# Kernel tuning notes

Hardware: AMD Instinct MI355X
Metric: run time of the kernel (lower is better)

Reference implementation:

```python
import jax, jax.numpy as jnp
import numpy as np
from jax import lax

BATCH, SEQ, D_FSQ = 8, 4096, 4
D_MODEL, D_STATE, D_CONV, L, OUT = 256, 16, 4, 2, 2
D_INNER = 2 * D_MODEL  # expand=2
EPS = 1e-5


def setup_inputs() -> dict:
    key = jax.random.key(0)
    ks = jax.random.split(key, 10)
    s = 0.02
    return {
        "z_seq": jax.random.normal(ks[0], (BATCH, SEQ, D_FSQ), jnp.float32),
        "ip_w": jax.random.normal(ks[1], (D_MODEL, D_FSQ), jnp.float32) * s,
        "ip_b": jnp.zeros((D_MODEL,), jnp.float32),
        "norm_g": jnp.ones((L, D_MODEL), jnp.float32),
        "norm_b": jnp.zeros((L, D_MODEL), jnp.float32),
        "inproj_w": jax.random.normal(ks[2], (L, 2 * D_INNER, D_MODEL), jnp.float32) * s,
        "conv_w": jax.random.normal(ks[3], (L, D_INNER, D_CONV), jnp.float32) * s,
        "conv_b": jnp.zeros((L, D_INNER), jnp.float32),
        "xproj_w": jax.random.normal(ks[4], (L, 2 * D_STATE + 1, D_INNER), jnp.float32) * s,
        "dt_w": jax.random.normal(ks[5], (L, D_INNER), jnp.float32) * s,
        "dt_b": jnp.zeros((L, D_INNER), jnp.float32),
        "outproj_w": jax.random.normal(ks[6], (L, D_MODEL, D_INNER), jnp.float32) * s,
        "onorm_g": jnp.ones((D_MODEL,), jnp.float32),
        "onorm_b": jnp.zeros((D_MODEL,), jnp.float32),
        "op_w": jax.random.normal(ks[7], (OUT, D_MODEL), jnp.float32) * s,
        "op_b": jnp.zeros((OUT,), jnp.float32),
    }


def _layernorm(x, g, b):
    mu = jnp.mean(x, axis=-1, keepdims=True)
    var = jnp.mean(jnp.square(x - mu), axis=-1, keepdims=True)
    return (x - mu) * lax.rsqrt(var + EPS) * g + b


def _selective_scan(x, dt, Bm, Cm):
    # x, dt: [B,T,d_inner]; Bm, Cm: [B,T,d_state]
    A = -jnp.arange(1, D_STATE + 1, dtype=x.dtype)  # [d_state]

    def step(h, inp):
        x_t, dt_t, B_t, C_t = inp  # [B,di],[B,di],[B,ds],[B,ds]
        A_bar = jnp.exp(dt_t[:, :, None] * A)            # [B,di,ds]
        h = A_bar * h + (dt_t * x_t)[:, :, None] * B_t[:, None, :]
        y_t = jnp.einsum("bds,bs->bd", h, C_t)
        return h, y_t

    xs = (jnp.swapaxes(x, 0, 1), jnp.swapaxes(dt, 0, 1),
          jnp.swapaxes(Bm, 0, 1), jnp.swapaxes(Cm, 0, 1))
    h0 = jnp.zeros((x.shape[0], D_INNER, D_STATE), x.dtype)
    _, ys = lax.scan(step, h0, xs)
    return jnp.swapaxes(ys, 0, 1)  # [B,T,d_inner]


def _block(x, g, b, Wi, cw, cb, Wx, dw, db, Wo):
    res = x
    x = _layernorm(x, g, b)
    xz = x @ Wi.T                               # [B,T,2*d_inner]
    xp, z = xz[..., :D_INNER], xz[..., D_INNER:]
    # causal depthwise conv1d (padding=d_conv-1 then truncate == left pad)
    xc = lax.conv_general_dilated(
        jnp.swapaxes(xp, 1, 2), cw[:, None, :], window_strides=(1,),
        padding=[(D_CONV - 1, 0)], dimension_numbers=("NCH", "OIH", "NCH"),
        feature_group_count=D_INNER) + cb[None, :, None]
    xc = jax.nn.silu(jnp.swapaxes(xc, 1, 2))    # [B,T,d_inner]
    ssm = xc @ Wx.T                             # [B,T,2*ds+1]
    Bm = ssm[..., :D_STATE]
    Cm = ssm[..., D_STATE:2 * D_STATE]
    dt_raw = ssm[..., 2 * D_STATE:]             # [B,T,1]
    dt = jax.nn.softplus(dt_raw * dw + db)      # Linear(1, d_inner)
    y = _selective_scan(xc, dt, Bm, Cm)
    y = y * jax.nn.silu(z)
    y = y @ Wo.T
    return y + res


def reference(z_seq, ip_w, ip_b, norm_g, norm_b, inproj_w, conv_w, conv_b,
              xproj_w, dt_w, dt_b, outproj_w, onorm_g, onorm_b, op_w, op_b):
    x = z_seq @ ip_w.T + ip_b
    for l in range(L):
        x = _block(x, norm_g[l], norm_b[l], inproj_w[l], conv_w[l], conv_b[l],
                   xproj_w[l], dt_w[l], dt_b[l], outproj_w[l])
    x = _layernorm(x, onorm_g, onorm_b)
    return x @ op_w.T + op_b
```

## Files before the change

kernel.cpp:

```cpp
#include <hip/hip_runtime.h>
#include <cstddef>
#include <cstdint>

#define DEV __device__ __forceinline__

namespace {
constexpr int BATCH = 8;
constexpr int SEQL  = 4096;
constexpr int DM    = 256;
constexpr int DS    = 16;
constexpr int DI    = 512;
constexpr int NTOK  = BATCH * SEQL;
constexpr int TC    = 32;
constexpr int NCH   = SEQL / TC;
constexpr float EPSF = 1e-5f;

constexpr size_t OFF_X   = 0;
constexpr size_t OFF_XPB = OFF_X   + (size_t)NTOK * DM * 4;
constexpr size_t OFF_ZBB = OFF_XPB + (size_t)NTOK * DI * 2;
constexpr size_t OFF_XCB = OFF_ZBB + (size_t)NTOK * DI * 2;
constexpr size_t OFF_XLN = OFF_XCB + (size_t)NTOK * DI * 2;
constexpr size_t OFF_B   = OFF_XLN + (size_t)NTOK * DM * 2;
constexpr size_t OFF_C   = OFF_B   + (size_t)NTOK * DS * 4;
constexpr size_t OFF_DTR = OFF_C   + (size_t)NTOK * DS * 4;
constexpr size_t OFF_HE  = OFF_DTR + (size_t)NTOK * 4;
constexpr size_t OFF_DTC = OFF_HE  + (size_t)BATCH * DI * NCH * DS * 4;
constexpr size_t OFF_WBI = OFF_DTC + (size_t)BATCH * DI * NCH * 4;
constexpr size_t OFF_WBO = OFF_WBI + (size_t)2 * 2 * DI * DM * 2;
constexpr size_t OFF_WBX = OFF_WBO + (size_t)2 * DM * DI * 2;
constexpr size_t OFF_CWT = OFF_WBX + (size_t)2 * 48 * DI * 2;
constexpr size_t WBI_EL  = 2 * 2 * DI * DM;
constexpr size_t WBO_EL  = 2 * DM * DI;
}

typedef __attribute__((ext_vector_type(8))) short short8;
typedef __attribute__((ext_vector_type(4))) float f32x4;

DEV float sigmoidf_(float v) { return 1.0f / (1.0f + __expf(-v)); }
DEV float siluf_(float v)    { return v * sigmoidf_(v); }
DEV float b2f(unsigned short u) {
    union { unsigned int i; float f; } c; c.i = ((unsigned int)u) << 16; return c.f;
}
DEV float4 b4f(ushort4 u) {
    return make_float4(b2f(u.x), b2f(u.y), b2f(u.z), b2f(u.w));
}
DEV unsigned short f2b(float f) {
    union { float f; unsigned int i; } c; c.f = f;
    unsigned int lsb = (c.i >> 16) & 1u;
    c.i += 0x7fffu + lsb;
    return (unsigned short)(c.i >> 16);
}
DEV void dt_p_(float a, float& dt, float& p) {
    p = __builtin_amdgcn_rcpf(1.0f + __expf(a));
    dt = -__logf(p);
}
DEV void pows16(float p, float* pb) {
    float p2 = p * p, p4 = p2 * p2, p8 = p4 * p4;
    pb[0] = p;        pb[1] = p2;       pb[2] = p2 * p;      pb[3] = p4;
    pb[4] = p4 * p;   pb[5] = p4 * p2;  pb[6] = p4 * p2 * p; pb[7] = p8;
    pb[8] = p8 * p;   pb[9] = p8 * p2;  pb[10] = p8 * p2 * p; pb[11] = p8 * p4;
    pb[12] = p8 * p4 * p; pb[13] = p8 * p4 * p2; pb[14] = p8 * p4 * p2 * p; pb[15] = p8 * p8;
}
DEV void gload_lds16(const unsigned short* g, unsigned short* l) {
    __builtin_amdgcn_global_load_lds(
        (__attribute__((address_space(1))) void*)(g),
        (__attribute__((address_space(3))) void*)(l), 16, 0, 0);
}

__global__ void k_cvt(const float* __restrict__ src, unsigned short* __restrict__ dst, int n) {
    int g = (blockIdx.x * 256 + threadIdx.x) * 4;
    if (g >= n) return;
    float4 v = *(const float4*)(src + g);
    ushort4 o;
    o.x = f2b(v.x); o.y = f2b(v.y); o.z = f2b(v.z); o.w = f2b(v.w);
    *(ushort4*)(dst + g) = o;
}

__global__ void k_cvtx(const float* __restrict__ src, unsigned short* __restrict__ dst) {
    int idx = blockIdx.x * 256 + threadIdx.x;
    int l = idx / (48 * 512), r = (idx >> 9) % 48, cc = idx & 511;
    dst[idx] = (r < 33) ? f2b(src[(size_t)(l * 33 + r) * 512 + cc]) : (unsigned short)0;
}

__global__ void k_cvtc(const float* __restrict__ src, float* __restrict__ dst) {
    int idx = blockIdx.x * 256 + threadIdx.x;
    int l = idx >> 11, k = (idx >> 9) & 3, d = idx & 511;
    dst[idx] = src[(size_t)(l * DI + d) * 4 + k];
}

__global__ void k_inproj(const float* __restrict__ z, const float* __restrict__ w,
                         const float* __restrict__ bias, float* __restrict__ x) {
    int g = blockIdx.x * 256 + threadIdx.x;
    int i = g >> 8, m = g & 255;
    float4 zv = *(const float4*)(z + (size_t)i * 4);
    float4 wv = *(const float4*)(w + (size_t)m * 4);
    float r = bias[m];
    r = fmaf(zv.x, wv.x, r);
    r = fmaf(zv.y, wv.y, r);
    r = fmaf(zv.z, wv.z, r);
    r = fmaf(zv.w, wv.w, r);
    x[g] = r;
}

__global__ void k_lnrow(const float* __restrict__ x, const float* __restrict__ gam,
                        const float* __restrict__ bet, unsigned short* __restrict__ xln) {
    int lane = threadIdx.x & 63, wid = threadIdx.x >> 6;
    int i = blockIdx.x * 4 + wid;
    float4 v = *(const float4*)(x + (size_t)i * DM + lane * 4);
    float s = v.x + v.y + v.z + v.w;
    float q = v.x * v.x + v.y * v.y + v.z * v.z + v.w * v.w;
    #pragma unroll
    for (int m = 32; m; m >>= 1) { s += __shfl_xor(s, m, 64); q += __shfl_xor(q, m, 64); }
    float mu = s * (1.0f / DM);
    float rs = rsqrtf(q * (1.0f / DM) - mu * mu + EPSF);
    float4 g4 = *(const float4*)(gam + lane * 4);
    float4 b4 = *(const float4*)(bet + lane * 4);
    ushort4 o;
    o.x = f2b((v.x - mu) * rs * g4.x + b4.x);
    o.y = f2b((v.y - mu) * rs * g4.y + b4.y);
    o.z = f2b((v.z - mu) * rs * g4.z + b4.z);
    o.w = f2b((v.w - mu) * rs * g4.w + b4.w);
    *(ushort4*)(xln + (size_t)i * DM + lane * 4) = o;
}

__global__ __launch_bounds__(256) void k_gemm1(
    const unsigned short* __restrict__ A, const unsigned short* __restrict__ W,
    unsigned short* __restrict__ xpb, unsigned short* __restrict__ zbb) {
    __shared__ unsigned short As[128 * 32];
    __shared__ unsigned short Bs[128 * 32];
    int tid = threadIdx.x, lane = tid & 63, wid = tid >> 6;
    int tileN = blockIdx.x & 7, tileM = blockIdx.x >> 3;
    int i0 = tileM * 128, n0 = tileN * 128;
    f32x4 acc[4][4];
    #pragma unroll
    for (int mi = 0; mi < 4; mi++)
        #pragma unroll
        for (int ni = 0; ni < 4; ni++) acc[mi][ni] = (f32x4){0.f, 0.f, 0.f, 0.f};

    int srow = (wid << 5) + (lane >> 2);
    int sblk = lane & 3;
    const unsigned short* ga = A + (size_t)(i0 + srow) * 256 + sblk * 8;
    const unsigned short* gb = W + (size_t)(n0 + srow) * 256 + sblk * 8;
    unsigned short* la = As + (wid << 5) * 32;
    unsigned short* lb = Bs + (wid << 5) * 32;
    int ar = lane & 15, ab = lane >> 4;
    const short8* pa = (const short8*)(As + ((wid >> 1) * 64 + ar) * 32 + ab * 8);
    const short8* pb = (const short8*)(Bs + ((wid & 1) * 64 + ar) * 32 + ab * 8);

    for (int k0 = 0; k0 < 256; k0 += 32) {
        gload_lds16(ga + k0,            la);
        gload_lds16(ga + k0 + 16 * 256, la + 16 * 32);
        gload_lds16(gb + k0,            lb);
        gload_lds16(gb + k0 + 16 * 256, lb + 16 * 32);
        __syncthreads();
        short8 a[4], b[4];
        #pragma unroll
        for (int mi = 0; mi < 4; mi++) a[mi] = pa[mi * 64];
        #pragma unroll
        for (int ni = 0; ni < 4; ni++) b[ni] = pb[ni * 64];
        #pragma unroll
        for (int mi = 0; mi < 4; mi++)
            #pragma unroll
            for (int ni = 0; ni < 4; ni++)
                acc[mi][ni] = __builtin_amdgcn_mfma_f32_16x16x32_bf16(a[mi], b[ni], acc[mi][ni], 0, 0, 0);
        __syncthreads();
    }
    int wr = wid >> 1, wc = wid & 1;
    int rbase = i0 + wr * 64 + (lane >> 4) * 4;
    int cbase = n0 + wc * 64 + (lane & 15);
    unsigned short* dst = (n0 < 512) ? xpb : zbb;
    int coff = (n0 < 512) ? cbase : cbase - 512;
    #pragma unroll
    for (int mi = 0; mi < 4; mi++)
        #pragma unroll
        for (int ni = 0; ni < 4; ni++)
            #pragma unroll
            for (int j = 0; j < 4; j++)
                dst[(size_t)(rbase + mi * 16 + j) * 512 + coff + ni * 16] = f2b(acc[mi][ni][j]);
}

__global__ void k_conv(const unsigned short* __restrict__ xpb, const float* __restrict__ cwT,
                       const float* __restrict__ cb, unsigned short* __restrict__ xcb) {
    int g = blockIdx.x * 256 + threadIdx.x;
    int tg = g >> 7, dq = g & 127;
    int d = dq * 4;
    int i0 = tg * 8;
    float4 w0 = *(const float4*)(cwT + 0 * DI + d);
    float4 w1 = *(const float4*)(cwT + 1 * DI + d);
    float4 w2 = *(const float4*)(cwT + 2 * DI + d);
    float4 w3 = *(const float4*)(cwT + 3 * DI + d);
    float4 bi = *(const float4*)(cb + d);
    float4 x0, x1, x2;
    if ((i0 & (SEQL - 1)) != 0) {
        x0 = b4f(*(const ushort4*)(xpb + (size_t)(i0 - 3) * DI + d));
        x1 = b4f(*(const ushort4*)(xpb + (size_t)(i0 - 2) * DI + d));
        x2 = b4f(*(const ushort4*)(xpb + (size_t)(i0 - 1) * DI + d));
    } else {
        x0 = x1 = x2 = make_float4(0.f, 0.f, 0.f, 0.f);
    }
    #pragma unroll
    for (int tt = 0; tt < 8; tt++) {
        float4 xc = b4f(*(const ushort4*)(xpb + (size_t)(i0 + tt) * DI + d));
        float4 a = bi;
        a.x = fmaf(w0.x, x0.x, a.x); a.y = fmaf(w0.y, x0.y, a.y);
        a.z = fmaf(w0.z, x0.z, a.z); a.w = fmaf(w0.w, x0.w, a.w);
        a.x = fmaf(w1.x, x1.x, a.x); a.y = fmaf(w1.y, x1.y, a.y);
        a.z = fmaf(w1.z, x1.z, a.z); a.w = fmaf(w1.w, x1.w, a.w);
        a.x = fmaf(w2.x, x2.x, a.x); a.y = fmaf(w2.y, x2.y, a.y);
        a.z = fmaf(w2.z, x2.z, a.z); a.w = fmaf(w2.w, x2.w, a.w);
        a.x = fmaf(w3.x, xc.x, a.x); a.y = fmaf(w3.y, xc.y, a.y);
        a.z = fmaf(w3.z, xc.z, a.z); a.w = fmaf(w3.w, xc.w, a.w);
        ushort4 o;
        o.x = f2b(siluf_(a.x)); o.y = f2b(siluf_(a.y));
        o.z = f2b(siluf_(a.z)); o.w = f2b(siluf_(a.w));
        *(ushort4*)(xcb + (size_t)(i0 + tt) * DI + d) = o;
        x0 = x1; x1 = x2; x2 = xc;
    }
}

__global__ __launch_bounds__(256) void k_xprojm(
    const unsigned short* __restrict__ A, const unsigned short* __restrict__ W,
    float* __restrict__ Bm, float* __restrict__ Cm, float* __restrict__ dtr) {
    __shared__ unsigned short As[128 * 32];
    __shared__ unsigned short Bs[48 * 32];
    int tid = threadIdx.x, lane = tid & 63, wid = tid >> 6;
    int i0 = blockIdx.x * 128;
    f32x4 acc[2][3];
    #pragma unroll
    for (int mi = 0; mi < 2; mi++)
        #pragma unroll
        for (int ni = 0; ni < 3; ni++) acc[mi][ni] = (f32x4){0.f, 0.f, 0.f, 0.f};

    int srow = lane >> 2, sblk = lane & 3;
    const unsigned short* ga = A + (size_t)(i0 + (wid << 5) + srow) * 512 + sblk * 8;
    unsigned short* la = As + (wid << 5) * 32;
    const unsigned short* gb = W + (size_t)((wid << 4) + srow) * 512 + sblk * 8;
    unsigned short* lb = Bs + (wid << 4) * 32;
    int ar = lane & 15, ab = lane >> 4;

    for (int k0 = 0; k0 < 512; k0 += 32) {
        gload_lds16(ga + k0,            la);
        gload_lds16(ga + k0 + 16 * 512, la + 16 * 32);
        if (wid < 3) gload_lds16(gb + k0, lb);
        __syncthreads();
        short8 a[2], b[3];
        #pragma unroll
        for (int mi = 0; mi < 2; mi++)
            a[mi] = *(const short8*)(As + ((wid << 5) + mi * 16 + ar) * 32 + ab * 8);
        #pragma unroll
        for (int ni = 0; ni < 3; ni++)
            b[ni] = *(const short8*)(Bs + (ni * 16 + ar) * 32 + ab * 8);
        #pragma unroll
        for (int mi = 0; mi < 2; mi++)
            #pragma unroll
            for (int ni = 0; ni < 3; ni++)
                acc[mi][ni] = __builtin_amdgcn_mfma_f32_16x16x32_bf16(a[mi], b[ni], acc[mi][ni], 0, 0, 0);
        __syncthreads();
    }
    #pragma unroll
    for (int mi = 0; mi < 2; mi++)
        #pragma unroll
        for (int ni = 0; ni < 3; ni++)
            #pragma unroll
            for (int j = 0; j < 4; j++) {
                int row = i0 + (wid << 5) + mi * 16 + (lane >> 4) * 4 + j;
                int ng = ni * 16 + (lane & 15);
                float v = acc[mi][ni][j];
                if (ng < 16)       Bm[(size_t)row * DS + ng] = v;
                else if (ng < 32)  Cm[(size_t)row * DS + ng - 16] = v;
                else if (ng == 32) dtr[row] = v;
            }
}

__global__ __launch_bounds__(256, 4) void k_scan1(
    const unsigned short* __restrict__ xcb, const float* __restrict__ Bm,
    const float* __restrict__ dtr, const float* __restrict__ dw,
    const float* __restrict__ db, float* __restrict__ hend, float* __restrict__ dtc) {
    __shared__ float Bsh[TC][16];
    __shared__ float dtl[TC];
    int tid = threadIdx.x;
    int blk = blockIdx.x;
    int c = blk & (NCH - 1), b = blk >> 7;
    int d0 = tid * 2;
    int i0 = (b << 12) + c * TC;
    if (tid < TC) dtl[tid] = dtr[i0 + tid];
    if (tid < TC * 4) {
        int tt = tid >> 2, ss = (tid & 3) * 4;
        *(float4*)(&Bsh[tt][ss]) = *(const float4*)(Bm + (size_t)(i0 + tt) * DS + ss);
    }
    __syncthreads();
    float2 dwd = *(const float2*)(dw + d0);
    float2 dbd = *(const float2*)(db + d0);
    float h0[16], h1[16];
    #pragma unroll
    for (int s = 0; s < 16; s++) { h0[s] = 0.0f; h1[s] = 0.0f; }
    float dts0 = 0.0f, dts1 = 0.0f;
    for (int t = 0; t < TC; t++) {
        float dt0, p0, dt1, p1;
        dt_p_(fmaf(dtl[t], dwd.x, dbd.x), dt0, p0);
        dt_p_(fmaf(dtl[t], dwd.y, dbd.y), dt1, p1);
        dts0 += dt0; dts1 += dt1;
        ushort2 xv = *(const ushort2*)(xcb + (size_t)(i0 + t) * DI + d0);
        float dtx0 = dt0 * b2f(xv.x);
        float dtx1 = dt1 * b2f(xv.y);
        float Bv[16];
        *(float4*)(Bv + 0)  = *(const float4*)(&Bsh[t][0]);
        *(float4*)(Bv + 4)  = *(const float4*)(&Bsh[t][4]);
        *(float4*)(Bv + 8)  = *(const float4*)(&Bsh[t][8]);
        *(float4*)(Bv + 12) = *(const float4*)(&Bsh[t][12]);
        float pb[16];
        pows16(p0, pb);
        #pragma unroll
        for (int s = 0; s < 16; s++) h0[s] = fmaf(pb[s], h0[s], dtx0 * Bv[s]);
        pows16(p1, pb);
        #pragma unroll
        for (int s = 0; s < 16; s++) h1[s] = fmaf(pb[s], h1[s], dtx1 * Bv[s]);
    }
    size_t hb0 = ((size_t)(b * DI + d0) * NCH + c) * DS;
    #pragma unroll
    for (int s = 0; s < 16; s += 4) {
        *(float4*)(hend + hb0 + s)      = make_float4(h0[s], h0[s+1], h0[s+2], h0[s+3]);
        *(float4*)(hend + hb0 + DS * NCH + s) = make_float4(h1[s], h1[s+1], h1[s+2], h1[s+3]);
    }
    dtc[(size_t)(b * DI + d0) * NCH + c] = dts0;
    dtc[(size_t)(b * DI + d0 + 1) * NCH + c] = dts1;
}

__global__ void k_scan2(float* __restrict__ hend, const float* __restrict__ dtc) {
    int g = blockIdx.x * 256 + threadIdx.x;
    int s = g & 15, dd = (g >> 4) & 511, b = g >> 13;
    size_t base = (size_t)(b * DI + dd) * NCH;
    float hin = 0.0f;
    float kneg = -(float)(s + 1);
    #pragma unroll 4
    for (int c = 0; c < NCH; c++) {
        size_t a = (base + c) * DS + s;
        float tmp = hend[a];
        float pb = __expf(kneg * dtc[base + c]);
        hend[a] = hin;
        hin = fmaf(pb, hin, tmp);
    }
}

__global__ __launch_bounds__(256, 4) void k_scan3(
    const unsigned short* __restrict__ xcb, const float* __restrict__ Bm,
    const float* __restrict__ Cm, const float* __restrict__ dtr,
    const float* __restrict__ dw, const float* __restrict__ db,
    const float* __restrict__ hend, const unsigned short* __restrict__ zbb,
    unsigned short* __restrict__ ygb) {
    __shared__ float Bsh[TC][16];
    __shared__ float Csh[TC][16];
    __shared__ float dtl[TC];
    int tid = threadIdx.x;
    int blk = blockIdx.x;
    int c = blk & (NCH - 1), b = blk >> 7;
    int d0 = tid * 2;
    int i0 = (b << 12) + c * TC;
    if (tid < TC) dtl[tid] = dtr[i0 + tid];
    if (tid < TC * 4) {
        int tt = tid >> 2, ss = (tid & 3) * 4;
        *(float4*)(&Bsh[tt][ss]) = *(const float4*)(Bm + (size_t)(i0 + tt) * DS + ss);
    } else if (tid < TC * 8) {
        int q = tid - TC * 4;
        int tt = q >> 2, ss = (q & 3) * 4;
        *(float4*)(&Csh[tt][ss]) = *(const float4*)(Cm + (size_t)(i0 + tt) * DS + ss);
    }
    __syncthreads();
    float2 dwd = *(const float2*)(dw + d0);
    float2 dbd = *(const float2*)(db + d0);
    float h0[16], h1[16];
    size_t hb0 = ((size_t)(b * DI + d0) * NCH + c) * DS;
    #pragma unroll
    for (int s = 0; s < 16; s += 4) {
        *(float4*)(h0 + s) = *(const float4*)(hend + hb0 + s);
        *(float4*)(h1 + s) = *(const float4*)(hend + hb0 + DS * NCH + s);
    }
    for (int t = 0; t < TC; t++) {
        float dt0, p0, dt1, p1;
        dt_p_(fmaf(dtl[t], dwd.x, dbd.x), dt0, p0);
        dt_p_(fmaf(dtl[t], dwd.y, dbd.y), dt1, p1);
        size_t gi = (size_t)(i0 + t) * DI + d0;
        ushort2 xv = *(const ushort2*)(xcb + gi);
        float dtx0 = dt0 * b2f(xv.x);
        float dtx1 = dt1 * b2f(xv.y);
        float Bv[16], Cv[16];
        *(float4*)(Bv + 0)  = *(const float4*)(&Bsh[t][0]);
        *(float4*)(Bv + 4)  = *(const float4*)(&Bsh[t][4]);
        *(float4*)(Bv + 8)  = *(const float4*)(&Bsh[t][8]);
        *(float4*)(Bv + 12) = *(const float4*)(&Bsh[t][12]);
        *(float4*)(Cv + 0)  = *(const float4*)(&Csh[t][0]);
        *(float4*)(Cv + 4)  = *(const float4*)(&Csh[t][4]);
        *(float4*)(Cv + 8)  = *(const float4*)(&Csh[t][8]);
        *(float4*)(Cv + 12) = *(const float4*)(&Csh[t][12]);
        float pb[16];
        float y0 = 0.0f, y1 = 0.0f;
        pows16(p0, pb);
        #pragma unroll
        for (int s = 0; s < 16; s++) {
            h0[s] = fmaf(pb[s], h0[s], dtx0 * Bv[s]);
            y0 = fmaf(h0[s], Cv[s], y0);
        }
        pows16(p1, pb);
        #pragma unroll
        for (int s = 0; s < 16; s++) {
            h1[s] = fmaf(pb[s], h1[s], dtx1 * Bv[s]);
            y1 = fmaf(h1[s], Cv[s], y1);
        }
        ushort2 zv = *(const ushort2*)(zbb + gi);
        ushort2 o;
        o.x = f2b(y0 * siluf_(b2f(zv.x)));
        o.y = f2b(y1 * siluf_(b2f(zv.y)));
        *(ushort2*)(ygb + gi) = o;
    }
}

__global__ __launch_bounds__(256) void k_outproj(
    const unsigned short* __restrict__ A, const unsigned short* __restrict__ W,
    float* __restrict__ x) {
    __shared__ unsigned short As[128 * 32];
    __shared__ unsigned short Bs[128 * 32];
    int tid = threadIdx.x, lane = tid & 63, wid = tid >> 6;
    int tileN = blockIdx.x & 1, tileM = blockIdx.x >> 1;
    int i0 = tileM * 128, n0 = tileN * 128;
    f32x4 acc[4][4];
    #pragma unroll
    for (int mi = 0; mi < 4; mi++)
        #pragma unroll
        for (int ni = 0; ni < 4; ni++) acc[mi][ni] = (f32x4){0.f, 0.f, 0.f, 0.f};

    int srow = (wid << 5) + (lane >> 2);
    int sblk = lane & 3;
    const unsigned short* ga = A + (size_t)(i0 + srow) * 512 + sblk * 8;
    const unsigned short* gb = W + (size_t)(n0 + srow) * 512 + sblk * 8;
    unsigned short* la = As + (wid << 5) * 32;
    unsigned short* lb = Bs + (wid << 5) * 32;
    int ar = lane & 15, ab = lane >> 4;
    const short8* pa = (const short8*)(As + ((wid >> 1) * 64 + ar) * 32 + ab * 8);
    const short8* pb = (const short8*)(Bs + ((wid & 1) * 64 + ar) * 32 + ab * 8);

    for (int k0 = 0; k0 < 512; k0 += 32) {
        gload_lds16(ga + k0,            la);
        gload_lds16(ga + k0 + 16 * 512, la + 16 * 32);
        gload_lds16(gb + k0,            lb);
        gload_lds16(gb + k0 + 16 * 512, lb + 16 * 32);
        __syncthreads();
        short8 a[4], b[4];
        #pragma unroll
        for (int mi = 0; mi < 4; mi++) a[mi] = pa[mi * 64];
        #pragma unroll
        for (int ni = 0; ni < 4; ni++) b[ni] = pb[ni * 64];
        #pragma unroll
        for (int mi = 0; mi < 4; mi++)
            #pragma unroll
            for (int ni = 0; ni < 4; ni++)
                acc[mi][ni] = __builtin_amdgcn_mfma_f32_16x16x32_bf16(a[mi], b[ni], acc[mi][ni], 0, 0, 0);
        __syncthreads();
    }
    int wr = wid >> 1, wc = wid & 1;
    int rbase = i0 + wr * 64 + (lane >> 4) * 4;
    int cbase = n0 + wc * 64 + (lane & 15);
    #pragma unroll
    for (int mi = 0; mi < 4; mi++)
        #pragma unroll
        for (int ni = 0; ni < 4; ni++)
            #pragma unroll
            for (int j = 0; j < 4; j++) {
                size_t idx = (size_t)(rbase + mi * 16 + j) * DM + cbase + ni * 16;
                x[idx] += acc[mi][ni][j];
            }
}

__global__ void k_final(const float* __restrict__ x, const float* __restrict__ gam,
                        const float* __restrict__ bet, const float* __restrict__ w,
                        const float* __restrict__ bias, float* __restrict__ out) {
    int lane = threadIdx.x & 63, wid = threadIdx.x >> 6;
    int i = blockIdx.x * 4 + wid;
    float4 v = *(const float4*)(x + (size_t)i * DM + lane * 4);
    float s = v.x + v.y + v.z + v.w;
    float q = v.x * v.x + v.y * v.y + v.z * v.z + v.w * v.w;
    #pragma unroll
    for (int m = 32; m; m >>= 1) { s += __shfl_xor(s, m, 64); q += __shfl_xor(q, m, 64); }
    float mu = s * (1.0f / DM);
    float rs = rsqrtf(q * (1.0f / DM) - mu * mu + EPSF);
    float4 gg = *(const float4*)(gam + lane * 4);
    float4 bb = *(const float4*)(bet + lane * 4);
    float xn[4] = {(v.x - mu) * rs * gg.x + bb.x, (v.y - mu) * rs * gg.y + bb.y,
                   (v.z - mu) * rs * gg.z + bb.z, (v.w - mu) * rs * gg.w + bb.w};
    float4 w0 = *(const float4*)(w + lane * 4);
    float4 w1 = *(const float4*)(w + DM + lane * 4);
    float p0 = xn[0] * w0.x + xn[1] * w0.y + xn[2] * w0.z + xn[3] * w0.w;
    float p1 = xn[0] * w1.x + xn[1] * w1.y + xn[2] * w1.z + xn[3] * w1.w;
    #pragma unroll
    for (int m = 32; m; m >>= 1) { p0 += __shfl_xor(p0, m, 64); p1 += __shfl_xor(p1, m, 64); }
    if (lane == 0) {
        out[(size_t)i * 2]     = p0 + bias[0];
        out[(size_t)i * 2 + 1] = p1 + bias[1];
    }
}

extern "C" void kernel_launch(void* const* d_in, const int* in_sizes, int n_in,
                              void* d_out, int out_size, void* d_ws, size_t ws_size,
                              hipStream_t stream) {
    const float* z_seq     = (const float*)d_in[0];
    const float* ip_w      = (const float*)d_in[1];
    const float* ip_b      = (const float*)d_in[2];
    const float* norm_g    = (const float*)d_in[3];
    const float* norm_b    = (const float*)d_in[4];
    const float* inproj_w  = (const float*)d_in[5];
    const float* conv_w    = (const float*)d_in[6];
    const float* conv_b    = (const float*)d_in[7];
    const float* xproj_w   = (const float*)d_in[8];
    const float* dt_w      = (const float*)d_in[9];
    const float* dt_b      = (const float*)d_in[10];
    const float* outproj_w = (const float*)d_in[11];
    const float* onorm_g   = (const float*)d_in[12];
    const float* onorm_b   = (const float*)d_in[13];
    const float* op_w      = (const float*)d_in[14];
    const float* op_b      = (const float*)d_in[15];

    char* ws = (char*)d_ws;
    float* x    = (float*)(ws + OFF_X);
    unsigned short* xpb = (unsigned short*)(ws + OFF_XPB);
    unsigned short* zbb = (unsigned short*)(ws + OFF_ZBB);
    unsigned short* xcb = (unsigned short*)(ws + OFF_XCB);
    unsigned short* xln = (unsigned short*)(ws + OFF_XLN);
    float* Bmb  = (float*)(ws + OFF_B);
    float* Cmb  = (float*)(ws + OFF_C);
    float* dtrb = (float*)(ws + OFF_DTR);
    float* hend = (float*)(ws + OFF_HE);
    float* dtc  = (float*)(ws + OFF_DTC);
    unsigned short* WbI = (unsigned short*)(ws + OFF_WBI);
    unsigned short* WbO = (unsigned short*)(ws + OFF_WBO);
    unsigned short* WbX = (unsigned short*)(ws + OFF_WBX);
    float* cwT  = (float*)(ws + OFF_CWT);

    k_cvt<<<(int)(WBI_EL / 4 / 256), 256, 0, stream>>>(inproj_w,  WbI, (int)WBI_EL);
    k_cvt<<<(int)(WBO_EL / 4 / 256), 256, 0, stream>>>(outproj_w, WbO, (int)WBO_EL);
    k_cvtx<<<2 * 48 * 512 / 256, 256, 0, stream>>>(xproj_w, WbX);
    k_cvtc<<<2 * 4 * 512 / 256, 256, 0, stream>>>(conv_w, cwT);

    k_inproj<<<NTOK * DM / 256, 256, 0, stream>>>(z_seq, ip_w, ip_b, x);

    for (int l = 0; l < 2; l++) {
        k_lnrow<<<NTOK / 4, 256, 0, stream>>>(x, norm_g + l * DM, norm_b + l * DM, xln);
        k_gemm1<<<(NTOK / 128) * 8, 256, 0, stream>>>(
            xln, WbI + (size_t)l * 2 * DI * DM, xpb, zbb);
        k_conv<<<(NTOK / 8) * 128 / 256, 256, 0, stream>>>(
            xpb, cwT + (size_t)l * 4 * DI, conv_b + (size_t)l * DI, xcb);
        k_xprojm<<<NTOK / 128, 256, 0, stream>>>(
            xcb, WbX + (size_t)l * 48 * DI, Bmb, Cmb, dtrb);
        k_scan1<<<BATCH * NCH, 256, 0, stream>>>(
            xcb, Bmb, dtrb, dt_w + l * DI, dt_b + l * DI, hend, dtc);
        k_scan2<<<BATCH * DI * DS / 256, 256, 0, stream>>>(hend, dtc);
        k_scan3<<<BATCH * NCH, 256, 0, stream>>>(
            xcb, Bmb, Cmb, dtrb, dt_w + l * DI, dt_b + l * DI, hend, zbb, xpb);
        k_outproj<<<(NTOK / 128) * 2, 256, 0, stream>>>(
            xpb, WbO + (size_t)l * DM * DI, x);
    }
    k_final<<<NTOK / 4, 256, 0, stream>>>(x, onorm_g, onorm_b, op_w, op_b, (float*)d_out);
}
```

Baseline: 547.2 us.

## Fuse weight prep kernels, fold first layernorm into inproj, split scan blocks

The four weight-conversion kernels are merged into one k_prep launch. The first-layer layernorm is computed inside k_inproj with a block-wide reduction, so the first k_lnrow pass over x is dropped. The scan1 and scan3 kernels now use 128-thread blocks, each covering half of the d_inner channels, which doubles the block count (2048) to raise occupancy and parallelism. The cost is that each half block reloads the same B/C/dt chunk into shared memory.

```diff
diff --git a/kernel.cpp b/kernel.cpp
--- a/kernel.cpp
+++ b/kernel.cpp
@@ -31,6 +31,10 @@
 constexpr size_t OFF_CWT = OFF_WBX + (size_t)2 * 48 * DI * 2;
 constexpr size_t WBI_EL  = 2 * 2 * DI * DM;
 constexpr size_t WBO_EL  = 2 * DM * DI;
+constexpr int PREP_T1 = (int)(WBI_EL / 4);
+constexpr int PREP_T2 = PREP_T1 + (int)(WBO_EL / 4);
+constexpr int PREP_T3 = PREP_T2 + 2 * 48 * 512;
+constexpr int PREP_T4 = PREP_T3 + 2 * 4 * 512;
 }
 
 typedef __attribute__((ext_vector_type(8))) short short8;
@@ -67,31 +71,45 @@
         (__attribute__((address_space(3))) void*)(l), 16, 0, 0);
 }
 
-__global__ void k_cvt(const float* __restrict__ src, unsigned short* __restrict__ dst, int n) {
-    int g = (blockIdx.x * 256 + threadIdx.x) * 4;
-    if (g >= n) return;
-    float4 v = *(const float4*)(src + g);
-    ushort4 o;
-    o.x = f2b(v.x); o.y = f2b(v.y); o.z = f2b(v.z); o.w = f2b(v.w);
-    *(ushort4*)(dst + g) = o;
-}
-
-__global__ void k_cvtx(const float* __restrict__ src, unsigned short* __restrict__ dst) {
+__global__ void k_prep(const float* __restrict__ inproj_w, const float* __restrict__ outproj_w,
+                       const float* __restrict__ xproj_w, const float* __restrict__ conv_w,
+                       unsigned short* __restrict__ WbI, unsigned short* __restrict__ WbO,
+                       unsigned short* __restrict__ WbX, float* __restrict__ cwT) {
     int idx = blockIdx.x * 256 + threadIdx.x;
-    int l = idx / (48 * 512), r = (idx >> 9) % 48, cc = idx & 511;
-    dst[idx] = (r < 33) ? f2b(src[(size_t)(l * 33 + r) * 512 + cc]) : (unsigned short)0;
-}
-
-__global__ void k_cvtc(const float* __restrict__ src, float* __restrict__ dst) {
-    int idx = blockIdx.x * 256 + threadIdx.x;
-    int l = idx >> 11, k = (idx >> 9) & 3, d = idx & 511;
-    dst[idx] = src[(size_t)(l * DI + d) * 4 + k];
-}
-
-__global__ void k_inproj(const float* __restrict__ z, const float* __restrict__ w,
-                         const float* __restrict__ bias, float* __restrict__ x) {
-    int g = blockIdx.x * 256 + threadIdx.x;
-    int i = g >> 8, m = g & 255;
+    if (idx < PREP_T1) {
+        int g = idx * 4;
+        float4 v = *(const float4*)(inproj_w + g);
+        ushort4 o; o.x = f2b(v.x); o.y = f2b(v.y); o.z = f2b(v.z); o.w = f2b(v.w);
+        *(ushort4*)(WbI + g) = o;
+        return;
+    }
+    if (idx < PREP_T2) {
+        int g = (idx - PREP_T1) * 4;
+        float4 v = *(const float4*)(outproj_w + g);
+        ushort4 o; o.x = f2b(v.x); o.y = f2b(v.y); o.z = f2b(v.z); o.w = f2b(v.w);
+        *(ushort4*)(WbO + g) = o;
+        return;
+    }
+    if (idx < PREP_T3) {
+        int q = idx - PREP_T2;
+        int l = q / (48 * 512), r = (q >> 9) % 48, cc = q & 511;
+        WbX[q] = (r < 33) ? f2b(xproj_w[(size_t)(l * 33 + r) * 512 + cc]) : (unsigned short)0;
+        return;
+    }
+    if (idx < PREP_T4) {
+        int q = idx - PREP_T3;
+        int l = q >> 11, k = (q >> 9) & 3, d = q & 511;
+        cwT[q] = conv_w[(size_t)(l * DI + d) * 4 + k];
+    }
+}
+
+__global__ __launch_bounds__(256) void k_inproj(
+    const float* __restrict__ z, const float* __restrict__ w,
+    const float* __restrict__ bias, const float* __restrict__ gam,
+    const float* __restrict__ bet, float* __restrict__ x,
+    unsigned short* __restrict__ xln) {
+    int i = blockIdx.x, m = threadIdx.x;
+    int lane = m & 63, wid = m >> 6;
     float4 zv = *(const float4*)(z + (size_t)i * 4);
     float4 wv = *(const float4*)(w + (size_t)m * 4);
     float r = bias[m];
@@ -99,7 +117,18 @@
     r = fmaf(zv.y, wv.y, r);
     r = fmaf(zv.z, wv.z, r);
     r = fmaf(zv.w, wv.w, r);
-    x[g] = r;
+    x[(size_t)i * DM + m] = r;
+    __shared__ float red[8];
+    float s = r, q = r * r;
+    #pragma unroll
+    for (int k = 32; k; k >>= 1) { s += __shfl_xor(s, k, 64); q += __shfl_xor(q, k, 64); }
+    if (lane == 0) { red[wid] = s; red[4 + wid] = q; }
+    __syncthreads();
+    float st = red[0] + red[1] + red[2] + red[3];
+    float qt = red[4] + red[5] + red[6] + red[7];
+    float mu = st * (1.0f / DM);
+    float rs = rsqrtf(qt * (1.0f / DM) - mu * mu + EPSF);
+    xln[(size_t)i * DM + m] = f2b((r - mu) * rs * gam[m] + bet[m]);
 }
 
 __global__ void k_lnrow(const float* __restrict__ x, const float* __restrict__ gam,
@@ -272,7 +301,7 @@
             }
 }
 
-__global__ __launch_bounds__(256, 4) void k_scan1(
+__global__ __launch_bounds__(128, 4) void k_scan1(
     const unsigned short* __restrict__ xcb, const float* __restrict__ Bm,
     const float* __restrict__ dtr, const float* __restrict__ dw,
     const float* __restrict__ db, float* __restrict__ hend, float* __restrict__ dtc) {
@@ -280,11 +309,11 @@
     __shared__ float dtl[TC];
     int tid = threadIdx.x;
     int blk = blockIdx.x;
-    int c = blk & (NCH - 1), b = blk >> 7;
-    int d0 = tid * 2;
+    int half = blk & 1, c = (blk >> 1) & (NCH - 1), b = blk >> 8;
+    int d0 = half * 256 + tid * 2;
     int i0 = (b << 12) + c * TC;
     if (tid < TC) dtl[tid] = dtr[i0 + tid];
-    if (tid < TC * 4) {
+    {
         int tt = tid >> 2, ss = (tid & 3) * 4;
         *(float4*)(&Bsh[tt][ss]) = *(const float4*)(Bm + (size_t)(i0 + tt) * DS + ss);
     }
@@ -319,8 +348,8 @@
     size_t hb0 = ((size_t)(b * DI + d0) * NCH + c) * DS;
     #pragma unroll
     for (int s = 0; s < 16; s += 4) {
-        *(float4*)(hend + hb0 + s)      = make_float4(h0[s], h0[s+1], h0[s+2], h0[s+3]);
-        *(float4*)(hend + hb0 + DS * NCH + s) = make_float4(h1[s], h1[s+1], h1[s+2], h1[s+3]);
+        *(float4*)(hend + hb0 + s) = make_float4(h0[s], h0[s+1], h0[s+2], h0[s+3]);
+        *(float4*)(hend + hb0 + (size_t)NCH * DS + s) = make_float4(h1[s], h1[s+1], h1[s+2], h1[s+3]);
     }
     dtc[(size_t)(b * DI + d0) * NCH + c] = dts0;
     dtc[(size_t)(b * DI + d0 + 1) * NCH + c] = dts1;
@@ -342,7 +371,7 @@
     }
 }
 
-__global__ __launch_bounds__(256, 4) void k_scan3(
+__global__ __launch_bounds__(128, 4) void k_scan3(
     const unsigned short* __restrict__ xcb, const float* __restrict__ Bm,
     const float* __restrict__ Cm, const float* __restrict__ dtr,
     const float* __restrict__ dw, const float* __restrict__ db,
@@ -353,16 +382,13 @@
     __shared__ float dtl[TC];
     int tid = threadIdx.x;
     int blk = blockIdx.x;
-    int c = blk & (NCH - 1), b = blk >> 7;
-    int d0 = tid * 2;
+    int half = blk & 1, c = (blk >> 1) & (NCH - 1), b = blk >> 8;
+    int d0 = half * 256 + tid * 2;
     int i0 = (b << 12) + c * TC;
     if (tid < TC) dtl[tid] = dtr[i0 + tid];
-    if (tid < TC * 4) {
+    {
         int tt = tid >> 2, ss = (tid & 3) * 4;
         *(float4*)(&Bsh[tt][ss]) = *(const float4*)(Bm + (size_t)(i0 + tt) * DS + ss);
-    } else if (tid < TC * 8) {
-        int q = tid - TC * 4;
-        int tt = q >> 2, ss = (q & 3) * 4;
         *(float4*)(&Csh[tt][ss]) = *(const float4*)(Cm + (size_t)(i0 + tt) * DS + ss);
     }
     __syncthreads();
@@ -373,7 +399,7 @@
     #pragma unroll
     for (int s = 0; s < 16; s += 4) {
         *(float4*)(h0 + s) = *(const float4*)(hend + hb0 + s);
-        *(float4*)(h1 + s) = *(const float4*)(hend + hb0 + DS * NCH + s);
+        *(float4*)(h1 + s) = *(const float4*)(hend + hb0 + (size_t)NCH * DS + s);
     }
     for (int t = 0; t < TC; t++) {
         float dt0, p0, dt1, p1;
@@ -534,25 +560,23 @@
     unsigned short* WbX = (unsigned short*)(ws + OFF_WBX);
     float* cwT  = (float*)(ws + OFF_CWT);
 
-    k_cvt<<<(int)(WBI_EL / 4 / 256), 256, 0, stream>>>(inproj_w,  WbI, (int)WBI_EL);
-    k_cvt<<<(int)(WBO_EL / 4 / 256), 256, 0, stream>>>(outproj_w, WbO, (int)WBO_EL);
-    k_cvtx<<<2 * 48 * 512 / 256, 256, 0, stream>>>(xproj_w, WbX);
-    k_cvtc<<<2 * 4 * 512 / 256, 256, 0, stream>>>(conv_w, cwT);
-
-    k_inproj<<<NTOK * DM / 256, 256, 0, stream>>>(z_seq, ip_w, ip_b, x);
+    k_prep<<<PREP_T4 / 256, 256, 0, stream>>>(inproj_w, outproj_w, xproj_w, conv_w,
+                                              WbI, WbO, WbX, cwT);
+    k_inproj<<<NTOK, 256, 0, stream>>>(z_seq, ip_w, ip_b, norm_g, norm_b, x, xln);
 
     for (int l = 0; l < 2; l++) {
-        k_lnrow<<<NTOK / 4, 256, 0, stream>>>(x, norm_g + l * DM, norm_b + l * DM, xln);
+        if (l > 0)
+            k_lnrow<<<NTOK / 4, 256, 0, stream>>>(x, norm_g + l * DM, norm_b + l * DM, xln);
         k_gemm1<<<(NTOK / 128) * 8, 256, 0, stream>>>(
             xln, WbI + (size_t)l * 2 * DI * DM, xpb, zbb);
         k_conv<<<(NTOK / 8) * 128 / 256, 256, 0, stream>>>(
             xpb, cwT + (size_t)l * 4 * DI, conv_b + (size_t)l * DI, xcb);
         k_xprojm<<<NTOK / 128, 256, 0, stream>>>(
             xcb, WbX + (size_t)l * 48 * DI, Bmb, Cmb, dtrb);
-        k_scan1<<<BATCH * NCH, 256, 0, stream>>>(
+        k_scan1<<<BATCH * NCH * 2, 128, 0, stream>>>(
             xcb, Bmb, dtrb, dt_w + l * DI, dt_b + l * DI, hend, dtc);
         k_scan2<<<BATCH * DI * DS / 256, 256, 0, stream>>>(hend, dtc);
-        k_scan3<<<BATCH * NCH, 256, 0, stream>>>(
+        k_scan3<<<BATCH * NCH * 2, 128, 0, stream>>>(
             xcb, Bmb, Cmb, dtrb, dt_w + l * DI, dt_b + l * DI, hend, zbb, xpb);
         k_outproj<<<(NTOK / 128) * 2, 256, 0, stream>>>(
             xpb, WbO + (size_t)l * DM * DI, x);
```

After: 531.6 us. 1.03x faster.
